# Kernel optimization log

Hardware: AMD Instinct MI355X
Metric: run time of the kernel (lower is better)

Reference implementation:

```python
import jax, jax.numpy as jnp
import numpy as np

N_NODES = 200000
N_EDGES = 6400000
IN_DIM = 15      # pfc_input_dim
POS_DIM = 4      # positional_dim
OUT_DIM = 2      # vtx_classes + 1


def setup_inputs() -> dict:
    key = jax.random.key(0)
    k1, k2, k3, k4, k5, k6, k7 = jax.random.split(key, 7)
    x_pfc = jax.random.normal(k1, (N_NODES, IN_DIM), dtype=jnp.float32)
    edge_index = jax.random.randint(k2, (2, N_EDGES), 0, N_NODES, dtype=jnp.int64)
    s_in = 1.0 / np.sqrt(IN_DIM)
    s_pos = 1.0 / np.sqrt(POS_DIM)
    # PointTransformerConv params: lin, lin_src, lin_dst (no bias), pos_nn = Linear(4, 2)
    W_lin = jax.random.uniform(k3, (OUT_DIM, IN_DIM), jnp.float32, -s_in, s_in)
    W_src = jax.random.uniform(k4, (OUT_DIM, IN_DIM), jnp.float32, -s_in, s_in)
    W_dst = jax.random.uniform(k5, (OUT_DIM, IN_DIM), jnp.float32, -s_in, s_in)
    W_pos = jax.random.uniform(k6, (OUT_DIM, POS_DIM), jnp.float32, -s_pos, s_pos)
    b_pos = jax.random.uniform(k7, (OUT_DIM,), jnp.float32, -s_pos, s_pos)
    return {"x_pfc": x_pfc, "edge_index": edge_index, "W_lin": W_lin,
            "W_src": W_src, "W_dst": W_dst, "W_pos": W_pos, "b_pos": b_pos}


def reference(x_pfc, edge_index, W_lin, W_src, W_dst, W_pos, b_pos):
    n = x_pfc.shape[0]
    pos = x_pfc[:, :POS_DIM]
    # original forward calls ptc_only(x, pos, edge_index.flip(0)):
    # source j = edge_index[1], target i = edge_index[0]
    j = edge_index[1]
    i = edge_index[0]
    # node-level linear maps (N x OUT_DIM)
    v = x_pfc @ W_lin.T
    a_src = x_pfc @ W_src.T
    a_dst = x_pfc @ W_dst.T
    # positional MLP on relative positions (E x OUT_DIM)
    delta = (pos[i] - pos[j]) @ W_pos.T + b_pos
    alpha = a_dst[i] - a_src[j] + delta
    # segment softmax over incoming edges of each target node i
    m = jax.ops.segment_max(alpha, i, num_segments=n)  # -inf for empty segments (never indexed)
    e = jnp.exp(alpha - m[i])
    denom = jax.ops.segment_sum(e, i, num_segments=n)
    attn = e / (denom[i] + 1e-16)
    msg = attn * (v[j] + delta)
    return jax.ops.segment_sum(msg, i, num_segments=n)
```

## Files before the change

### kernel.cpp

```cpp
#include <hip/hip_runtime.h>

#define N_NODES 200000
#define N_EDGES 6400000
#define IN_DIM 15
#define POS_DIM 4

#define CSHIFT 8
#define CMASK 255
#define CW 256
#define NCOARSE ((N_NODES + CW - 1) >> CSHIFT)
#define CHUNK 8192
#define NBLK ((N_EDGES + CHUNK - 1) / CHUNK)
#define CAP 9216

typedef unsigned uv4 __attribute__((ext_vector_type(4)));

__global__ void node_prep(const float* __restrict__ x,
                          const float* __restrict__ Wlin,
                          const float* __restrict__ Wsrc,
                          const float* __restrict__ Wdst,
                          const float* __restrict__ Wpos,
                          float2* __restrict__ tabI,
                          float4* __restrict__ tabJ,
                          float2* __restrict__ pvec)
{
    int n = blockIdx.x * blockDim.x + threadIdx.x;
    if (n >= N_NODES) return;
    const float* xp = x + (long)n * IN_DIM;
    float xv[IN_DIM];
#pragma unroll
    for (int k = 0; k < IN_DIM; ++k) xv[k] = xp[k];

    float p0 = 0.f, p1 = 0.f;
#pragma unroll
    for (int k = 0; k < POS_DIM; ++k) {
        p0 += Wpos[k] * xv[k];
        p1 += Wpos[POS_DIM + k] * xv[k];
    }
    float v0 = 0.f, v1 = 0.f, as0 = 0.f, as1 = 0.f, ad0 = 0.f, ad1 = 0.f;
#pragma unroll
    for (int k = 0; k < IN_DIM; ++k) {
        float xk = xv[k];
        v0  += Wlin[k] * xk;           v1  += Wlin[IN_DIM + k] * xk;
        as0 += Wsrc[k] * xk;           as1 += Wsrc[IN_DIM + k] * xk;
        ad0 += Wdst[k] * xk;           ad1 += Wdst[IN_DIM + k] * xk;
    }
    tabI[n] = make_float2(ad0 + p0, ad1 + p1);
    tabJ[n] = make_float4(as0 + p0, as1 + p1, v0 - p0, v1 - p1);
    pvec[n] = make_float2(p0, p1);
}

__global__ void hist_kernel(const int* __restrict__ idx,
                            unsigned* __restrict__ hist)
{
    __shared__ unsigned h[NCOARSE];
    for (int t = threadIdx.x; t < NCOARSE; t += blockDim.x) h[t] = 0u;
    __syncthreads();
    long s0 = (long)blockIdx.x * CHUNK;
    int end = (int)min((long)CHUNK, (long)N_EDGES - s0);
    for (int t = threadIdx.x * 4; t < end; t += 2048) {
        int4 iv = *(const int4*)(idx + s0 + t);
        atomicAdd(&h[iv.x >> CSHIFT], 1u);
        atomicAdd(&h[iv.y >> CSHIFT], 1u);
        atomicAdd(&h[iv.z >> CSHIFT], 1u);
        atomicAdd(&h[iv.w >> CSHIFT], 1u);
    }
    __syncthreads();
    for (int t = threadIdx.x; t < NCOARSE; t += blockDim.x)
        hist[(unsigned)blockIdx.x * NCOARSE + t] = h[t];
}

__global__ void colscan_kernel(unsigned* __restrict__ hist,
                               unsigned* __restrict__ totals)
{
    __shared__ unsigned s[1024];
    int k = blockIdx.x;
    int t = threadIdx.x;
    int e0 = t, e1 = t + 512;
    unsigned v0 = (e0 < NBLK) ? hist[(unsigned)e0 * NCOARSE + k] : 0u;
    unsigned v1 = (e1 < NBLK) ? hist[(unsigned)e1 * NCOARSE + k] : 0u;
    s[e0] = v0; s[e1] = v1;
    __syncthreads();
    for (int o = 1; o < 1024; o <<= 1) {
        unsigned a0 = (e0 >= o) ? s[e0 - o] : 0u;
        unsigned a1 = (e1 >= o) ? s[e1 - o] : 0u;
        __syncthreads();
        s[e0] += a0; s[e1] += a1;
        __syncthreads();
    }
    if (e0 < NBLK) hist[(unsigned)e0 * NCOARSE + k] = s[e0] - v0;
    if (e1 < NBLK) hist[(unsigned)e1 * NCOARSE + k] = s[e1] - v1;
    if (e1 == NBLK - 1) totals[k] = s[e1];
}

__global__ void basescan_kernel(const unsigned* __restrict__ totals,
                                unsigned* __restrict__ base)
{
    __shared__ unsigned s[1024];
    int t = threadIdx.x;
    int e0 = t, e1 = t + 512;
    unsigned v0 = (e0 < NCOARSE) ? ((totals[e0] + 3u) & ~3u) : 0u;
    unsigned v1 = (e1 < NCOARSE) ? ((totals[e1] + 3u) & ~3u) : 0u;
    s[e0] = v0; s[e1] = v1;
    __syncthreads();
    for (int off = 1; off < 1024; off <<= 1) {
        unsigned a0 = (e0 >= off) ? s[e0 - off] : 0u;
        unsigned a1 = (e1 >= off) ? s[e1 - off] : 0u;
        __syncthreads();
        s[e0] += a0; s[e1] += a1;
        __syncthreads();
    }
    if (e0 < NCOARSE) base[e0] = s[e0] - v0;
    if (e1 < NCOARSE) base[e1] = s[e1] - v1;
}

__global__ void scatter_kernel(const int* __restrict__ idx,
                               const unsigned* __restrict__ hist,
                               const unsigned* __restrict__ base,
                               unsigned* __restrict__ packed)
{
    __shared__ unsigned stage[CHUNK];
    __shared__ unsigned cnt[1024];
    __shared__ unsigned gdst[1024];
    int b = blockIdx.x;
    int t = threadIdx.x;
    long s0 = (long)b * CHUNK;
    int end = (int)min((long)CHUNK, (long)N_EDGES - s0);
    cnt[t] = 0u; cnt[t + 512] = 0u;
    __syncthreads();
    for (int e = t * 4; e < end; e += 2048) {
        int4 iv = *(const int4*)(idx + s0 + e);
        atomicAdd(&cnt[iv.x >> CSHIFT], 1u);
        atomicAdd(&cnt[iv.y >> CSHIFT], 1u);
        atomicAdd(&cnt[iv.z >> CSHIFT], 1u);
        atomicAdd(&cnt[iv.w >> CSHIFT], 1u);
    }
    __syncthreads();
    unsigned c0 = cnt[t], c1 = cnt[t + 512];
    for (int o = 1; o < 1024; o <<= 1) {
        unsigned a0 = (t >= o) ? cnt[t - o] : 0u;
        unsigned a1 = (t + 512 >= o) ? cnt[t + 512 - o] : 0u;
        __syncthreads();
        cnt[t] += a0; cnt[t + 512] += a1;
        __syncthreads();
    }
    unsigned ex0 = cnt[t] - c0;
    unsigned ex1 = cnt[t + 512] - c1;
    if (t < NCOARSE) gdst[t] = base[t] + hist[(unsigned)b * NCOARSE + t];
    {
        int u = t + 512;
        if (u < NCOARSE) gdst[u] = base[u] + hist[(unsigned)b * NCOARSE + u];
    }
    __syncthreads();
    cnt[t] = ex0; cnt[t + 512] = ex1;
    __syncthreads();
    for (int e = t * 4; e < end; e += 2048) {
        int4 iv = *(const int4*)(idx + s0 + e);
        int4 jv = *(const int4*)(idx + N_EDGES + s0 + e);
        unsigned r0 = atomicAdd(&cnt[iv.x >> CSHIFT], 1u);
        unsigned r1 = atomicAdd(&cnt[iv.y >> CSHIFT], 1u);
        unsigned r2 = atomicAdd(&cnt[iv.z >> CSHIFT], 1u);
        unsigned r3 = atomicAdd(&cnt[iv.w >> CSHIFT], 1u);
        stage[r0] = ((unsigned)jv.x << CSHIFT) | (unsigned)(iv.x & CMASK);
        stage[r1] = ((unsigned)jv.y << CSHIFT) | (unsigned)(iv.y & CMASK);
        stage[r2] = ((unsigned)jv.z << CSHIFT) | (unsigned)(iv.z & CMASK);
        stage[r3] = ((unsigned)jv.w << CSHIFT) | (unsigned)(iv.w & CMASK);
    }
    __syncthreads();
    int g = t >> 4, l = t & 15;
    for (int bk = g; bk < 1024; bk += 32) {
        unsigned st = bk ? cnt[bk - 1] : 0u;
        unsigned len = cnt[bk] - st;
        if (len == 0u) continue;
        unsigned gd = gdst[bk];
        for (unsigned e = l; e < len; e += 16u)
            packed[gd + e] = stage[st + e];
    }
}

__global__ void bucket_agg_kernel(const unsigned* __restrict__ packed,
                                  const unsigned* __restrict__ base,
                                  const unsigned* __restrict__ totals,
                                  const float2* __restrict__ tabI,
                                  const float4* __restrict__ tabJ,
                                  const float2* __restrict__ pvec,
                                  const float* __restrict__ bpos,
                                  float2* __restrict__ out)
{
    __shared__ unsigned cache[CAP + 256];
    __shared__ unsigned cnt[256], sc[256], cur[256];
    int k = blockIdx.x;
    int t = threadIdx.x;
    unsigned s = base[k];
    unsigned n = min(totals[k], (unsigned)CAP);
    if (t < 256) cnt[t] = 0u;
    __syncthreads();
    for (unsigned e = 4u * t; e < n; e += 2048u) {
        uv4 p = *(const uv4*)(packed + s + e);
        atomicAdd(&cnt[p.x & CMASK], 1u);
        if (e + 1 < n) atomicAdd(&cnt[p.y & CMASK], 1u);
        if (e + 2 < n) atomicAdd(&cnt[p.z & CMASK], 1u);
        if (e + 3 < n) atomicAdd(&cnt[p.w & CMASK], 1u);
    }
    __syncthreads();
    if (t < 256) sc[t] = cnt[t];
    __syncthreads();
    for (int o = 1; o < 256; o <<= 1) {
        unsigned a = 0u;
        if (t < 256 && t >= o) a = sc[t - o];
        __syncthreads();
        if (t < 256) sc[t] += a;
        __syncthreads();
    }
    if (t < 256) cur[t] = sc[t] - cnt[t] + (unsigned)t;
    __syncthreads();
    for (unsigned e = 4u * t; e < n; e += 2048u) {
        uv4 p = __builtin_nontemporal_load((const uv4*)(packed + s + e));
        { unsigned pos = atomicAdd(&cur[p.x & CMASK], 1u); cache[pos] = p.x >> CSHIFT; }
        if (e + 1 < n) { unsigned pos = atomicAdd(&cur[p.y & CMASK], 1u); cache[pos] = p.y >> CSHIFT; }
        if (e + 2 < n) { unsigned pos = atomicAdd(&cur[p.z & CMASK], 1u); cache[pos] = p.z >> CSHIFT; }
        if (e + 3 < n) { unsigned pos = atomicAdd(&cur[p.w & CMASK], 1u); cache[pos] = p.w >> CSHIFT; }
    }
    __syncthreads();
    int m = t >> 1, q = t & 1;
    int gn = (k << CSHIFT) + m;
    if (gn >= N_NODES) return;
    unsigned deg = cnt[m];
    unsigned st  = sc[m] - deg + (unsigned)m;
    unsigned h   = (deg >> 1) & ~3u;
    unsigned lo  = q ? h : 0u, hi = q ? deg : h;
    float b0 = bpos[0], b1 = bpos[1];
    float2 fi = tabI[gn];
    float a0 = fi.x + b0, a1 = fi.y + b1;
    float sn0 = 0.f, sn1 = 0.f, sd0 = 0.f, sd1 = 0.f;
    unsigned e = lo;
    for (; e + 4u <= hi; e += 4u) {
        unsigned j0 = cache[st + e],     j1 = cache[st + e + 1];
        unsigned j2 = cache[st + e + 2], j3 = cache[st + e + 3];
        float4 f0 = tabJ[j0], f1 = tabJ[j1], f2 = tabJ[j2], f3 = tabJ[j3];
        float e00 = __expf(a0 - f0.x), e01 = __expf(a1 - f0.y);
        float e10 = __expf(a0 - f1.x), e11 = __expf(a1 - f1.y);
        float e20 = __expf(a0 - f2.x), e21 = __expf(a1 - f2.y);
        float e30 = __expf(a0 - f3.x), e31 = __expf(a1 - f3.y);
        sn0 += e00 * f0.z + e10 * f1.z + e20 * f2.z + e30 * f3.z;
        sn1 += e01 * f0.w + e11 * f1.w + e21 * f2.w + e31 * f3.w;
        sd0 += e00 + e10 + e20 + e30;
        sd1 += e01 + e11 + e21 + e31;
    }
    for (; e < hi; ++e) {
        unsigned j = cache[st + e];
        float4 fj = tabJ[j];
        float e0 = __expf(a0 - fj.x), e1 = __expf(a1 - fj.y);
        sn0 += e0 * fj.z;  sn1 += e1 * fj.w;
        sd0 += e0;         sd1 += e1;
    }
    sn0 += __shfl_xor(sn0, 1);
    sn1 += __shfl_xor(sn1, 1);
    sd0 += __shfl_xor(sd0, 1);
    sd1 += __shfl_xor(sd1, 1);
    if (q == 0) {
        float2 p = pvec[gn];
        float o0 = (sn0 + (p.x + b0) * sd0) / (sd0 + 1e-16f);
        float o1 = (sn1 + (p.y + b1) * sd1) / (sd1 + 1e-16f);
        out[gn] = make_float2(o0, o1);
    }
}

extern "C" void kernel_launch(void* const* d_in, const int* in_sizes, int n_in,
                              void* d_out, int out_size, void* d_ws, size_t ws_size,
                              hipStream_t stream) {
    const float* x    = (const float*)d_in[0];
    const int*   idx  = (const int*)d_in[1];
    const float* Wlin = (const float*)d_in[2];
    const float* Wsrc = (const float*)d_in[3];
    const float* Wdst = (const float*)d_in[4];
    const float* Wpos = (const float*)d_in[5];
    const float* bpos = (const float*)d_in[6];
    float* out = (float*)d_out;

    char* ws = (char*)d_ws;
    size_t off = 0;
    float4* tabJ = (float4*)(ws + off); off += (size_t)N_NODES * 16;
    float2* tabI = (float2*)(ws + off); off += (size_t)N_NODES * 8;
    float2* pvec = (float2*)(ws + off); off += (size_t)N_NODES * 8;
    unsigned* packed = (unsigned*)(ws + off); off += ((size_t)N_EDGES + 4u * NCOARSE) * 4;
    unsigned* hist   = (unsigned*)(ws + off); off += (size_t)NBLK * NCOARSE * 4;
    unsigned* totals = (unsigned*)(ws + off); off += (size_t)NCOARSE * 4;
    unsigned* base   = (unsigned*)(ws + off); off += (size_t)NCOARSE * 4;

    node_prep<<<(N_NODES + 255) / 256, 256, 0, stream>>>(x, Wlin, Wsrc, Wdst, Wpos,
                                                         tabI, tabJ, pvec);
    hist_kernel<<<NBLK, 512, 0, stream>>>(idx, hist);
    colscan_kernel<<<NCOARSE, 512, 0, stream>>>(hist, totals);
    basescan_kernel<<<1, 512, 0, stream>>>(totals, base);
    scatter_kernel<<<NBLK, 512, 0, stream>>>(idx, hist, base, packed);
    bucket_agg_kernel<<<NCOARSE, 512, 0, stream>>>(packed, base, totals,
                                                   tabI, tabJ, pvec, bpos,
                                                   (float2*)out);
}
```

Baseline: 183.3 us.

## Replace per-bucket LDS counting sort with direct LDS float atomic accumulation

The aggregation kernel no longer counts, prefix-sums and scatters source indices into a sorted LDS cache before a per-node gather loop. Each thread now streams packed edges, gathers the tabJ entry, computes the exponentials and adds numerator and denominator terms into per-node LDS float accumulators with atomics. This drops two passes over the packed data, several barriers and the CAP truncation. In exchange it adds four LDS float atomics per edge, with contention on nodes that have many incoming edges, and the summation order becomes nondeterministic.

```diff
diff --git a/kernel.cpp b/kernel.cpp
--- a/kernel.cpp
+++ b/kernel.cpp
@@ -11,7 +11,6 @@
 #define NCOARSE ((N_NODES + CW - 1) >> CSHIFT)
 #define CHUNK 8192
 #define NBLK ((N_EDGES + CHUNK - 1) / CHUNK)
-#define CAP 9216
 
 typedef unsigned uv4 __attribute__((ext_vector_type(4)));
 
@@ -187,82 +186,55 @@
                                   const float* __restrict__ bpos,
                                   float2* __restrict__ out)
 {
-    __shared__ unsigned cache[CAP + 256];
-    __shared__ unsigned cnt[256], sc[256], cur[256];
+    __shared__ float acc[1024];
+    __shared__ float2 ti[256];
     int k = blockIdx.x;
     int t = threadIdx.x;
     unsigned s = base[k];
-    unsigned n = min(totals[k], (unsigned)CAP);
-    if (t < 256) cnt[t] = 0u;
-    __syncthreads();
-    for (unsigned e = 4u * t; e < n; e += 2048u) {
-        uv4 p = *(const uv4*)(packed + s + e);
-        atomicAdd(&cnt[p.x & CMASK], 1u);
-        if (e + 1 < n) atomicAdd(&cnt[p.y & CMASK], 1u);
-        if (e + 2 < n) atomicAdd(&cnt[p.z & CMASK], 1u);
-        if (e + 3 < n) atomicAdd(&cnt[p.w & CMASK], 1u);
-    }
-    __syncthreads();
-    if (t < 256) sc[t] = cnt[t];
-    __syncthreads();
-    for (int o = 1; o < 256; o <<= 1) {
-        unsigned a = 0u;
-        if (t < 256 && t >= o) a = sc[t - o];
-        __syncthreads();
-        if (t < 256) sc[t] += a;
-        __syncthreads();
-    }
-    if (t < 256) cur[t] = sc[t] - cnt[t] + (unsigned)t;
+    unsigned n = totals[k];
+    float b0 = bpos[0], b1 = bpos[1];
+    acc[t] = 0.f; acc[t + 512] = 0.f;
+    if (t < 256) {
+        int gn = (k << CSHIFT) + t;
+        float2 fi = (gn < N_NODES) ? tabI[gn] : make_float2(0.f, 0.f);
+        ti[t] = make_float2(fi.x + b0, fi.y + b1);
+    }
     __syncthreads();
     for (unsigned e = 4u * t; e < n; e += 2048u) {
         uv4 p = __builtin_nontemporal_load((const uv4*)(packed + s + e));
-        { unsigned pos = atomicAdd(&cur[p.x & CMASK], 1u); cache[pos] = p.x >> CSHIFT; }
-        if (e + 1 < n) { unsigned pos = atomicAdd(&cur[p.y & CMASK], 1u); cache[pos] = p.y >> CSHIFT; }
-        if (e + 2 < n) { unsigned pos = atomicAdd(&cur[p.z & CMASK], 1u); cache[pos] = p.z >> CSHIFT; }
-        if (e + 3 < n) { unsigned pos = atomicAdd(&cur[p.w & CMASK], 1u); cache[pos] = p.w >> CSHIFT; }
-    }
-    __syncthreads();
-    int m = t >> 1, q = t & 1;
-    int gn = (k << CSHIFT) + m;
-    if (gn >= N_NODES) return;
-    unsigned deg = cnt[m];
-    unsigned st  = sc[m] - deg + (unsigned)m;
-    unsigned h   = (deg >> 1) & ~3u;
-    unsigned lo  = q ? h : 0u, hi = q ? deg : h;
-    float b0 = bpos[0], b1 = bpos[1];
-    float2 fi = tabI[gn];
-    float a0 = fi.x + b0, a1 = fi.y + b1;
-    float sn0 = 0.f, sn1 = 0.f, sd0 = 0.f, sd1 = 0.f;
-    unsigned e = lo;
-    for (; e + 4u <= hi; e += 4u) {
-        unsigned j0 = cache[st + e],     j1 = cache[st + e + 1];
-        unsigned j2 = cache[st + e + 2], j3 = cache[st + e + 3];
-        float4 f0 = tabJ[j0], f1 = tabJ[j1], f2 = tabJ[j2], f3 = tabJ[j3];
-        float e00 = __expf(a0 - f0.x), e01 = __expf(a1 - f0.y);
-        float e10 = __expf(a0 - f1.x), e11 = __expf(a1 - f1.y);
-        float e20 = __expf(a0 - f2.x), e21 = __expf(a1 - f2.y);
-        float e30 = __expf(a0 - f3.x), e31 = __expf(a1 - f3.y);
-        sn0 += e00 * f0.z + e10 * f1.z + e20 * f2.z + e30 * f3.z;
-        sn1 += e01 * f0.w + e11 * f1.w + e21 * f2.w + e31 * f3.w;
-        sd0 += e00 + e10 + e20 + e30;
-        sd1 += e01 + e11 + e21 + e31;
-    }
-    for (; e < hi; ++e) {
-        unsigned j = cache[st + e];
-        float4 fj = tabJ[j];
-        float e0 = __expf(a0 - fj.x), e1 = __expf(a1 - fj.y);
-        sn0 += e0 * fj.z;  sn1 += e1 * fj.w;
-        sd0 += e0;         sd1 += e1;
-    }
-    sn0 += __shfl_xor(sn0, 1);
-    sn1 += __shfl_xor(sn1, 1);
-    sd0 += __shfl_xor(sd0, 1);
-    sd1 += __shfl_xor(sd1, 1);
-    if (q == 0) {
-        float2 p = pvec[gn];
-        float o0 = (sn0 + (p.x + b0) * sd0) / (sd0 + 1e-16f);
-        float o1 = (sn1 + (p.y + b1) * sd1) / (sd1 + 1e-16f);
-        out[gn] = make_float2(o0, o1);
+        unsigned pe[4] = {p.x, p.y, p.z, p.w};
+        bool ok[4]; int lo[4]; float4 fj[4];
+#pragma unroll
+        for (int c = 0; c < 4; ++c) {
+            ok[c] = (e + (unsigned)c) < n;
+            lo[c] = (int)(pe[c] & CMASK);
+            int j = ok[c] ? (int)(pe[c] >> CSHIFT) : 0;
+            fj[c] = tabJ[j];
+        }
+#pragma unroll
+        for (int c = 0; c < 4; ++c) {
+            float2 f = ti[lo[c]];
+            float e0 = __expf(f.x - fj[c].x);
+            float e1 = __expf(f.y - fj[c].y);
+            if (ok[c]) {
+                atomicAdd(&acc[lo[c]],       e0 * fj[c].z);
+                atomicAdd(&acc[256 + lo[c]], e1 * fj[c].w);
+                atomicAdd(&acc[512 + lo[c]], e0);
+                atomicAdd(&acc[768 + lo[c]], e1);
+            }
+        }
+    }
+    __syncthreads();
+    if (t < 256) {
+        int gn = (k << CSHIFT) + t;
+        if (gn < N_NODES) {
+            float sn0 = acc[t],       sn1 = acc[256 + t];
+            float sd0 = acc[512 + t], sd1 = acc[768 + t];
+            float2 p = pvec[gn];
+            float o0 = (sn0 + (p.x + b0) * sd0) / (sd0 + 1e-16f);
+            float o1 = (sn1 + (p.y + b1) * sd1) / (sd1 + 1e-16f);
+            out[gn] = make_float2(o0, o1);
+        }
     }
 }
 
```

After: 316.1 us. +72.4%, slower.
